# Performance work log

Hardware: AMD Instinct MI355X
Metric: run time of the kernel (lower is better)

The kernel has to match this reference:

```python
import jax, jax.numpy as jnp
import numpy as np

D_IN, D_MODEL = 512, 256
B, N = 2, 512


def setup_inputs() -> dict:
    key = jax.random.key(0)
    ks = jax.random.split(key, 8)
    xav_x = float(np.sqrt(2.0 / (D_IN + D_MODEL)))
    xav_p = float(np.sqrt(2.0 / (4 + D_MODEL)))
    return {
        "x": jax.random.normal(ks[0], (B, N, D_IN), dtype=jnp.float32),
        "pos": jax.random.normal(ks[1], (B, N, 4), dtype=jnp.float32),
        "attn_mask": jax.random.randint(ks[2], (B, N, N), 0, 2, dtype=jnp.int32),
        "Wx": jax.random.normal(ks[3], (D_IN, D_MODEL), dtype=jnp.float32) * xav_x,
        "bx": jnp.zeros((D_MODEL,), dtype=jnp.float32),
        "Wp": jax.random.normal(ks[4], (4, D_MODEL), dtype=jnp.float32) * xav_p,
        "bp": jnp.zeros((D_MODEL,), dtype=jnp.float32),
        "w": jax.random.normal(ks[5], (D_MODEL,), dtype=jnp.float32) * 0.05,
    }


def reference(x, pos, attn_mask, Wx, bx, Wp, bp, w):
    # projected, activated inputs: [B, N, d_model]
    h = jnp.tanh(x @ Wx + bx)
    # pairwise relative positions: [B, N, N, 4]
    rel = pos[:, :, None, :] - pos[:, None, :, :]
    # position MLP + tanh: [B, N, N, d_model]
    z = jnp.tanh(rel @ Wp + bp)
    # scores via dot with weight vector: [B, N, N]
    attn = jnp.einsum("bijd,d->bij", z, w)
    mask = attn_mask != 0
    attn = jnp.where(mask, attn, -jnp.inf)
    attn = jax.nn.softmax(attn, axis=2)
    attn = jnp.where(mask, attn, 0.0)
    # dropout is identity in eval mode
    # weighted sum: [B, N, d_model]
    output = jnp.einsum("bij,bjd->bid", attn, h)
    return (output, attn)
```

## Files before the change

### kernel.cpp

```cpp
#include <hip/hip_runtime.h>
#include <hip/hip_bf16.h>
#include <math.h>

#define BATCH   2
#define SEQ     512
#define DIN     512
#define DM      256

#define LOG2E2  2.88539008177792681f

#if __has_builtin(__builtin_amdgcn_exp2f)
#define EXP2(x) __builtin_amdgcn_exp2f(x)
#else
#define EXP2(x) exp2f(x)
#endif
#if __has_builtin(__builtin_amdgcn_rcpf)
#define RCP(x) __builtin_amdgcn_rcpf(x)
#else
#define RCP(x) (1.0f / (x))
#endif

__device__ __forceinline__ float tanh_from_scaled(float targ) {
    return fmaf(-2.0f, RCP(1.0f + EXP2(targ)), 1.0f);
}

__global__ __launch_bounds__(512) void produce_k(
    const float* __restrict__ pos,
    const float* __restrict__ Wp,
    const float* __restrict__ x,
    const float* __restrict__ Wx,
    const float* __restrict__ bx,
    float4* __restrict__ EB4,
    float* __restrict__ h)
{
    const int tid = threadIdx.x;

    if (blockIdx.x < 128) {
        const int b  = blockIdx.x >> 6;
        const int q  = blockIdx.x & 63;
        const int d0 = 4 * q;
        const float4 p = ((const float4*)pos)[b * SEQ + tid];
        float e[4];
        #pragma unroll
        for (int i = 0; i < 4; i++) {
            const int d = d0 + i;
            const float P = fmaf(p.x, Wp[d], fmaf(p.y, Wp[DM + d],
                            fmaf(p.z, Wp[2*DM + d], p.w * Wp[3*DM + d])));
            e[i] = EXP2(-LOG2E2 * P);
        }
        EB4[((size_t)(b * 64 + q)) * SEQ + tid] = make_float4(e[0], e[1], e[2], e[3]);
        return;
    }

    __shared__ float s_xt[32][68];
    __shared__ float s_wt[64][64];

    const int idx = blockIdx.x - 128;
    const int rt  = idx >> 2;
    const int ct  = idx & 3;
    const int ty  = tid >> 4;
    const int tx  = tid & 15;
    const int row = rt * 32 + ty;
    const int dcol = ct * 64 + 4 * tx;

    float4 acc = make_float4(0.f, 0.f, 0.f, 0.f);

    for (int ks = 0; ks < 8; ks++) {
        const int k0 = ks * 64;
        {
            const int r = tid >> 4, c = tid & 15;
            *(float4*)&s_xt[r][4 * c] =
                *(const float4*)(x + (size_t)(rt * 32 + r) * DIN + k0 + 4 * c);
        }
        #pragma unroll
        for (int s = 0; s < 2; s++) {
            const int fidx = s * 512 + tid;
            const int r = fidx >> 4, c = fidx & 15;
            *(float4*)&s_wt[r][4 * c] =
                *(const float4*)(Wx + (size_t)(k0 + r) * DM + ct * 64 + 4 * c);
        }
        __syncthreads();

        #pragma unroll 8
        for (int k = 0; k < 64; k++) {
            const float  xv = s_xt[ty][k];
            const float4 wq = *(const float4*)&s_wt[k][4 * tx];
            acc.x = fmaf(xv, wq.x, acc.x);
            acc.y = fmaf(xv, wq.y, acc.y);
            acc.z = fmaf(xv, wq.z, acc.z);
            acc.w = fmaf(xv, wq.w, acc.w);
        }
        __syncthreads();
    }

    const float4 bq = *(const float4*)(bx + dcol);
    float4 t;
    t.x = tanh_from_scaled(LOG2E2 * (acc.x + bq.x));
    t.y = tanh_from_scaled(LOG2E2 * (acc.y + bq.y));
    t.z = tanh_from_scaled(LOG2E2 * (acc.z + bq.z));
    t.w = tanh_from_scaled(LOG2E2 * (acc.w + bq.w));
    *(float4*)(h + (size_t)row * DM + dcol) = t;
}

__global__ __launch_bounds__(512) void attend_k(
    const float* __restrict__ pos,
    const float* __restrict__ Wp,
    const float* __restrict__ bp,
    const int*   __restrict__ mask,
    const float* __restrict__ wv,
    const float4* __restrict__ EB4,
    const float* __restrict__ h,
    float* __restrict__ out,
    float* __restrict__ attn_out)
{
    const int b   = blockIdx.x >> 8;
    const int i0  = (blockIdx.x & 255) * 2;
    const int tid = threadIdx.x;
    const int l   = tid & 63;

    __shared__ float4 s_eaA[64], s_eaB[64];
    __shared__ float  s_p[2][SEQ];
    __shared__ float  s_red[2][8];
    __shared__ float  s_o[7][2][DM];

    {
        const int rr = __builtin_amdgcn_readfirstlane(tid >> 8);
        const int d  = tid & 255;
        const float4 p = ((const float4*)pos)[b * SEQ + i0 + rr];
        const float P = fmaf(p.x, Wp[d],
                        fmaf(p.y, Wp[DM + d],
                        fmaf(p.z, Wp[2*DM + d],
                             p.w * Wp[3*DM + d])));
        const float ea = EXP2(LOG2E2 * (P + bp[d]));
        ((float*)(rr ? s_eaB : s_eaA))[d] = ea;
    }
    __syncthreads();

    const float4* __restrict__ EBj = EB4 + (size_t)b * 64 * SEQ + tid;

    float aA = 0.f, aB = 0.f;
    #pragma unroll 8
    for (int q = 0; q < 64; q++) {
        const float4 eb = EBj[(size_t)q * SEQ];
        const float4 eA = s_eaA[q];
        const float4 eB = s_eaB[q];
        const float4 wq = *(const float4*)(wv + 4 * q);

        const float yA0 = fmaf(eA.x, eb.x, 1.0f);
        const float yA1 = fmaf(eA.y, eb.y, 1.0f);
        const float yA2 = fmaf(eA.z, eb.z, 1.0f);
        const float yA3 = fmaf(eA.w, eb.w, 1.0f);
        aA = fmaf(fmaf(wq.y, yA0, wq.x * yA1), RCP(yA0 * yA1), aA);
        aA = fmaf(fmaf(wq.w, yA2, wq.z * yA3), RCP(yA2 * yA3), aA);

        const float yB0 = fmaf(eB.x, eb.x, 1.0f);
        const float yB1 = fmaf(eB.y, eb.y, 1.0f);
        const float yB2 = fmaf(eB.z, eb.z, 1.0f);
        const float yB3 = fmaf(eB.w, eb.w, 1.0f);
        aB = fmaf(fmaf(wq.y, yB0, wq.x * yB1), RCP(yB0 * yB1), aB);
        aB = fmaf(fmaf(wq.w, yB2, wq.z * yB3), RCP(yB2 * yB3), aB);
    }

    const size_t mrowA = (size_t)b * SEQ * SEQ + (size_t)i0 * SEQ + tid;
    const int mA = mask[mrowA];
    const int mB = mask[mrowA + SEQ];
    float pA = mA ? EXP2(-LOG2E2 * aA) : 0.f;
    float pB = mB ? EXP2(-LOG2E2 * aB) : 0.f;

    float sA = pA, sB = pB;
    #pragma unroll
    for (int off = 32; off; off >>= 1) {
        sA += __shfl_xor(sA, off, 64);
        sB += __shfl_xor(sB, off, 64);
    }
    if (l == 0) { s_red[0][tid >> 6] = sA; s_red[1][tid >> 6] = sB; }
    __syncthreads();

    const float4 ra = ((const float4*)s_red[0])[0], rb = ((const float4*)s_red[0])[1];
    const float4 rc = ((const float4*)s_red[1])[0], rd = ((const float4*)s_red[1])[1];
    pA *= __fdividef(1.0f, (ra.x+ra.y+ra.z+ra.w) + (rb.x+rb.y+rb.z+rb.w));
    pB *= __fdividef(1.0f, (rc.x+rc.y+rc.z+rc.w) + (rd.x+rd.y+rd.z+rd.w));

    attn_out[mrowA]       = pA;
    attn_out[mrowA + SEQ] = pB;
    s_p[0][tid] = pA;
    s_p[1][tid] = pB;
    __syncthreads();

    const int dq = tid & 63;
    const int js = __builtin_amdgcn_readfirstlane(tid >> 6);
    const float* __restrict__ hp = h + (size_t)(b * SEQ + js * 64) * DM + 4 * dq;
    const float* __restrict__ p0 = &s_p[0][js * 64];
    const float* __restrict__ p1 = &s_p[1][js * 64];

    float4 a0 = make_float4(0,0,0,0), a1 = a0;
    #pragma unroll 4
    for (int jj = 0; jj < 16; jj++) {
        const float4 P0 = *(const float4*)(p0 + 4 * jj);
        const float4 P1 = *(const float4*)(p1 + 4 * jj);
        const float4 h0 = *(const float4*)(hp + (size_t)(4*jj + 0) * DM);
        const float4 h1 = *(const float4*)(hp + (size_t)(4*jj + 1) * DM);
        const float4 h2 = *(const float4*)(hp + (size_t)(4*jj + 2) * DM);
        const float4 h3 = *(const float4*)(hp + (size_t)(4*jj + 3) * DM);

        a0.x = fmaf(P0.x,h0.x,fmaf(P0.y,h1.x,fmaf(P0.z,h2.x,fmaf(P0.w,h3.x,a0.x))));
        a0.y = fmaf(P0.x,h0.y,fmaf(P0.y,h1.y,fmaf(P0.z,h2.y,fmaf(P0.w,h3.y,a0.y))));
        a0.z = fmaf(P0.x,h0.z,fmaf(P0.y,h1.z,fmaf(P0.z,h2.z,fmaf(P0.w,h3.z,a0.z))));
        a0.w = fmaf(P0.x,h0.w,fmaf(P0.y,h1.w,fmaf(P0.z,h2.w,fmaf(P0.w,h3.w,a0.w))));
        a1.x = fmaf(P1.x,h0.x,fmaf(P1.y,h1.x,fmaf(P1.z,h2.x,fmaf(P1.w,h3.x,a1.x))));
        a1.y = fmaf(P1.x,h0.y,fmaf(P1.y,h1.y,fmaf(P1.z,h2.y,fmaf(P1.w,h3.y,a1.y))));
        a1.z = fmaf(P1.x,h0.z,fmaf(P1.y,h1.z,fmaf(P1.z,h2.z,fmaf(P1.w,h3.z,a1.z))));
        a1.w = fmaf(P1.x,h0.w,fmaf(P1.y,h1.w,fmaf(P1.z,h2.w,fmaf(P1.w,h3.w,a1.w))));
    }

    if (js > 0) {
        *(float4*)&s_o[js - 1][0][4 * dq] = a0;
        *(float4*)&s_o[js - 1][1][4 * dq] = a1;
    }
    __syncthreads();
    if (js == 0) {
        #pragma unroll
        for (int s = 0; s < 7; s++) {
            const float4 q0 = *(const float4*)&s_o[s][0][4 * dq];
            const float4 q1 = *(const float4*)&s_o[s][1][4 * dq];
            a0.x += q0.x; a0.y += q0.y; a0.z += q0.z; a0.w += q0.w;
            a1.x += q1.x; a1.y += q1.y; a1.z += q1.z; a1.w += q1.w;
        }
        float* __restrict__ op = out + (size_t)(b * SEQ + i0) * DM + 4 * dq;
        *(float4*)(op)      = a0;
        *(float4*)(op + DM) = a1;
    }
}

extern "C" void kernel_launch(void* const* d_in, const int* in_sizes, int n_in,
                              void* d_out, int out_size, void* d_ws, size_t ws_size,
                              hipStream_t stream) {
    const float* x    = (const float*)d_in[0];
    const float* pos  = (const float*)d_in[1];
    const int*   mask = (const int*)  d_in[2];
    const float* Wx   = (const float*)d_in[3];
    const float* bx   = (const float*)d_in[4];
    const float* Wp   = (const float*)d_in[5];
    const float* bp   = (const float*)d_in[6];
    const float* wv   = (const float*)d_in[7];

    float* out      = (float*)d_out;
    float* attn_out = (float*)d_out + (size_t)BATCH*SEQ*DM;

    char*   ws  = (char*)d_ws;
    float*  h   = (float*)(ws);
    float4* EB4 = (float4*)(ws + (size_t)BATCH*SEQ*DM*4);

    produce_k<<<256, 512, 0, stream>>>(pos, Wp, x, Wx, bx, EB4, h);
    attend_k <<<(BATCH*SEQ)/2, 512, 0, stream>>>(pos, Wp, bp, mask, wv, EB4, h, out, attn_out);
}
```

Baseline: 114.8 us.

## Process four query rows per block and split Wx GEMM along K

The attend kernel now handles four query rows per block instead of two. Each EB value loaded from global memory is reused across four rows, which halves the number of blocks and halves the global traffic for EB and h. The EB layout changes from float4 per feature group to a scalar per feature, and the inner loop pairs adjacent features differently. The h GEMM in produce_k splits K across two half-blocks with a shared-memory reduction and uses narrower 32-column tiles, giving 256 GEMM blocks instead of 128. The cost is more registers and shared memory per attend block and fewer attend blocks (256) available to fill the GPU.

After: 106.8 us (median of 2 runs). 7.0% less time.

```diff
diff --git a/kernel.cpp b/kernel.cpp
--- a/kernel.cpp
+++ b/kernel.cpp
@@ -30,7 +30,7 @@
     const float* __restrict__ x,
     const float* __restrict__ Wx,
     const float* __restrict__ bx,
-    float4* __restrict__ EB4,
+    float* __restrict__ EBf,
     float* __restrict__ h)
 {
     const int tid = threadIdx.x;
@@ -40,51 +40,53 @@
         const int q  = blockIdx.x & 63;
         const int d0 = 4 * q;
         const float4 p = ((const float4*)pos)[b * SEQ + tid];
-        float e[4];
         #pragma unroll
         for (int i = 0; i < 4; i++) {
             const int d = d0 + i;
             const float P = fmaf(p.x, Wp[d], fmaf(p.y, Wp[DM + d],
                             fmaf(p.z, Wp[2*DM + d], p.w * Wp[3*DM + d])));
-            e[i] = EXP2(-LOG2E2 * P);
-        }
-        EB4[((size_t)(b * 64 + q)) * SEQ + tid] = make_float4(e[0], e[1], e[2], e[3]);
+            EBf[((size_t)(b * DM + d)) * SEQ + tid] = EXP2(-LOG2E2 * P);
+        }
         return;
     }
 
-    __shared__ float s_xt[32][68];
-    __shared__ float s_wt[64][64];
+    __shared__ float  s_xt[2][32][68];
+    __shared__ float  s_wt[2][64][32];
+    __shared__ float4 s_part[256];
 
     const int idx = blockIdx.x - 128;
-    const int rt  = idx >> 2;
-    const int ct  = idx & 3;
-    const int ty  = tid >> 4;
-    const int tx  = tid & 15;
+    const int rt  = idx >> 3;
+    const int ct  = idx & 7;
+    const int kh  = __builtin_amdgcn_readfirstlane(tid >> 8);
+    const int t   = tid & 255;
+    const int ty  = t >> 3;
+    const int tx  = t & 7;
     const int row = rt * 32 + ty;
-    const int dcol = ct * 64 + 4 * tx;
 
     float4 acc = make_float4(0.f, 0.f, 0.f, 0.f);
 
-    for (int ks = 0; ks < 8; ks++) {
-        const int k0 = ks * 64;
-        {
-            const int r = tid >> 4, c = tid & 15;
-            *(float4*)&s_xt[r][4 * c] =
-                *(const float4*)(x + (size_t)(rt * 32 + r) * DIN + k0 + 4 * c);
-        }
+    for (int ks = 0; ks < 4; ks++) {
+        const int k0 = kh * 256 + ks * 64;
         #pragma unroll
         for (int s = 0; s < 2; s++) {
-            const int fidx = s * 512 + tid;
+            const int fidx = t * 2 + s;
             const int r = fidx >> 4, c = fidx & 15;
-            *(float4*)&s_wt[r][4 * c] =
-                *(const float4*)(Wx + (size_t)(k0 + r) * DM + ct * 64 + 4 * c);
+            *(float4*)&s_xt[kh][r][4 * c] =
+                *(const float4*)(x + (size_t)(rt * 32 + r) * DIN + k0 + 4 * c);
+        }
+        #pragma unroll
+        for (int s = 0; s < 2; s++) {
+            const int fidx = t * 2 + s;
+            const int r = fidx >> 3, c = fidx & 7;
+            *(float4*)&s_wt[kh][r][4 * c] =
+                *(const float4*)(Wx + (size_t)(k0 + r) * DM + ct * 32 + 4 * c);
         }
         __syncthreads();
 
         #pragma unroll 8
         for (int k = 0; k < 64; k++) {
-            const float  xv = s_xt[ty][k];
-            const float4 wq = *(const float4*)&s_wt[k][4 * tx];
+            const float  xv = s_xt[kh][ty][k];
+            const float4 wq = *(const float4*)&s_wt[kh][k][4 * tx];
             acc.x = fmaf(xv, wq.x, acc.x);
             acc.y = fmaf(xv, wq.y, acc.y);
             acc.z = fmaf(xv, wq.z, acc.z);
@@ -93,13 +95,18 @@
         __syncthreads();
     }
 
-    const float4 bq = *(const float4*)(bx + dcol);
-    float4 t;
-    t.x = tanh_from_scaled(LOG2E2 * (acc.x + bq.x));
-    t.y = tanh_from_scaled(LOG2E2 * (acc.y + bq.y));
-    t.z = tanh_from_scaled(LOG2E2 * (acc.z + bq.z));
-    t.w = tanh_from_scaled(LOG2E2 * (acc.w + bq.w));
-    *(float4*)(h + (size_t)row * DM + dcol) = t;
+    if (kh == 1) s_part[t] = acc;
+    __syncthreads();
+    if (kh == 0) {
+        const float4 q4 = s_part[t];
+        const float4 bq = *(const float4*)(bx + ct * 32 + 4 * tx);
+        float4 o;
+        o.x = tanh_from_scaled(LOG2E2 * (acc.x + q4.x + bq.x));
+        o.y = tanh_from_scaled(LOG2E2 * (acc.y + q4.y + bq.y));
+        o.z = tanh_from_scaled(LOG2E2 * (acc.z + q4.z + bq.z));
+        o.w = tanh_from_scaled(LOG2E2 * (acc.w + q4.w + bq.w));
+        *(float4*)(h + (size_t)row * DM + ct * 32 + 4 * tx) = o;
+    }
 }
 
 __global__ __launch_bounds__(512) void attend_k(
@@ -108,114 +115,150 @@
     const float* __restrict__ bp,
     const int*   __restrict__ mask,
     const float* __restrict__ wv,
-    const float4* __restrict__ EB4,
+    const float* __restrict__ EBf,
     const float* __restrict__ h,
     float* __restrict__ out,
     float* __restrict__ attn_out)
 {
-    const int b   = blockIdx.x >> 8;
-    const int i0  = (blockIdx.x & 255) * 2;
+    const int b   = blockIdx.x >> 7;
+    const int i0  = (blockIdx.x & 127) * 4;
     const int tid = threadIdx.x;
     const int l   = tid & 63;
 
-    __shared__ float4 s_eaA[64], s_eaB[64];
-    __shared__ float  s_p[2][SEQ];
-    __shared__ float  s_red[2][8];
-    __shared__ float  s_o[7][2][DM];
+    __shared__ float4 s_ea[DM];
+    __shared__ float  s_p[4][SEQ];
+    __shared__ float  s_red[4][8];
+    __shared__ float  s_o[7][4][DM];
 
     {
-        const int rr = __builtin_amdgcn_readfirstlane(tid >> 8);
         const int d  = tid & 255;
-        const float4 p = ((const float4*)pos)[b * SEQ + i0 + rr];
-        const float P = fmaf(p.x, Wp[d],
-                        fmaf(p.y, Wp[DM + d],
-                        fmaf(p.z, Wp[2*DM + d],
-                             p.w * Wp[3*DM + d])));
-        const float ea = EXP2(LOG2E2 * (P + bp[d]));
-        ((float*)(rr ? s_eaB : s_eaA))[d] = ea;
-    }
-    __syncthreads();
-
-    const float4* __restrict__ EBj = EB4 + (size_t)b * 64 * SEQ + tid;
-
-    float aA = 0.f, aB = 0.f;
+        const int rp = __builtin_amdgcn_readfirstlane(tid >> 8);
+        const int r0 = rp * 2;
+        const float4 p0 = ((const float4*)pos)[b * SEQ + i0 + r0];
+        const float4 p1 = ((const float4*)pos)[b * SEQ + i0 + r0 + 1];
+        const float wp0 = Wp[d], wp1 = Wp[DM + d], wp2 = Wp[2*DM + d], wp3 = Wp[3*DM + d];
+        const float bpd = bp[d];
+        const float P0 = fmaf(p0.x, wp0, fmaf(p0.y, wp1, fmaf(p0.z, wp2, p0.w * wp3)));
+        const float P1 = fmaf(p1.x, wp0, fmaf(p1.y, wp1, fmaf(p1.z, wp2, p1.w * wp3)));
+        float* se = (float*)&s_ea[d];
+        se[r0]     = EXP2(LOG2E2 * (P0 + bpd));
+        se[r0 + 1] = EXP2(LOG2E2 * (P1 + bpd));
+    }
+    __syncthreads();
+
+    const float* __restrict__ EBj = EBf + (size_t)b * DM * SEQ + tid;
+
+    float a0 = 0.f, a1 = 0.f, a2 = 0.f, a3 = 0.f;
     #pragma unroll 8
-    for (int q = 0; q < 64; q++) {
-        const float4 eb = EBj[(size_t)q * SEQ];
-        const float4 eA = s_eaA[q];
-        const float4 eB = s_eaB[q];
-        const float4 wq = *(const float4*)(wv + 4 * q);
-
-        const float yA0 = fmaf(eA.x, eb.x, 1.0f);
-        const float yA1 = fmaf(eA.y, eb.y, 1.0f);
-        const float yA2 = fmaf(eA.z, eb.z, 1.0f);
-        const float yA3 = fmaf(eA.w, eb.w, 1.0f);
-        aA = fmaf(fmaf(wq.y, yA0, wq.x * yA1), RCP(yA0 * yA1), aA);
-        aA = fmaf(fmaf(wq.w, yA2, wq.z * yA3), RCP(yA2 * yA3), aA);
-
-        const float yB0 = fmaf(eB.x, eb.x, 1.0f);
-        const float yB1 = fmaf(eB.y, eb.y, 1.0f);
-        const float yB2 = fmaf(eB.z, eb.z, 1.0f);
-        const float yB3 = fmaf(eB.w, eb.w, 1.0f);
-        aB = fmaf(fmaf(wq.y, yB0, wq.x * yB1), RCP(yB0 * yB1), aB);
-        aB = fmaf(fmaf(wq.w, yB2, wq.z * yB3), RCP(yB2 * yB3), aB);
-    }
-
-    const size_t mrowA = (size_t)b * SEQ * SEQ + (size_t)i0 * SEQ + tid;
-    const int mA = mask[mrowA];
-    const int mB = mask[mrowA + SEQ];
-    float pA = mA ? EXP2(-LOG2E2 * aA) : 0.f;
-    float pB = mB ? EXP2(-LOG2E2 * aB) : 0.f;
-
-    float sA = pA, sB = pB;
+    for (int t = 0; t < 128; t++) {
+        const float eb0 = EBj[(size_t)(2*t) * SEQ];
+        const float eb1 = EBj[(size_t)(2*t + 1) * SEQ];
+        const float4 eA = s_ea[2*t];
+        const float4 eB = s_ea[2*t + 1];
+        const float w0 = wv[2*t];
+        const float w1 = wv[2*t + 1];
+
+        {
+            const float y0 = fmaf(eA.x, eb0, 1.f), y1 = fmaf(eB.x, eb1, 1.f);
+            a0 = fmaf(fmaf(w0, y1, w1 * y0), RCP(y0 * y1), a0);
+        }
+        {
+            const float y0 = fmaf(eA.y, eb0, 1.f), y1 = fmaf(eB.y, eb1, 1.f);
+            a1 = fmaf(fmaf(w0, y1, w1 * y0), RCP(y0 * y1), a1);
+        }
+        {
+            const float y0 = fmaf(eA.z, eb0, 1.f), y1 = fmaf(eB.z, eb1, 1.f);
+            a2 = fmaf(fmaf(w0, y1, w1 * y0), RCP(y0 * y1), a2);
+        }
+        {
+            const float y0 = fmaf(eA.w, eb0, 1.f), y1 = fmaf(eB.w, eb1, 1.f);
+            a3 = fmaf(fmaf(w0, y1, w1 * y0), RCP(y0 * y1), a3);
+        }
+    }
+
+    const size_t mrow = (size_t)b * SEQ * SEQ + (size_t)i0 * SEQ + tid;
+    const int m0 = mask[mrow];
+    const int m1 = mask[mrow + SEQ];
+    const int m2 = mask[mrow + 2*SEQ];
+    const int m3 = mask[mrow + 3*SEQ];
+    float p0 = m0 ? EXP2(-LOG2E2 * a0) : 0.f;
+    float p1 = m1 ? EXP2(-LOG2E2 * a1) : 0.f;
+    float p2 = m2 ? EXP2(-LOG2E2 * a2) : 0.f;
+    float p3 = m3 ? EXP2(-LOG2E2 * a3) : 0.f;
+
+    float s0 = p0, s1 = p1, s2 = p2, s3 = p3;
     #pragma unroll
     for (int off = 32; off; off >>= 1) {
-        sA += __shfl_xor(sA, off, 64);
-        sB += __shfl_xor(sB, off, 64);
-    }
-    if (l == 0) { s_red[0][tid >> 6] = sA; s_red[1][tid >> 6] = sB; }
-    __syncthreads();
-
-    const float4 ra = ((const float4*)s_red[0])[0], rb = ((const float4*)s_red[0])[1];
-    const float4 rc = ((const float4*)s_red[1])[0], rd = ((const float4*)s_red[1])[1];
-    pA *= __fdividef(1.0f, (ra.x+ra.y+ra.z+ra.w) + (rb.x+rb.y+rb.z+rb.w));
-    pB *= __fdividef(1.0f, (rc.x+rc.y+rc.z+rc.w) + (rd.x+rd.y+rd.z+rd.w));
-
-    attn_out[mrowA]       = pA;
-    attn_out[mrowA + SEQ] = pB;
-    s_p[0][tid] = pA;
-    s_p[1][tid] = pB;
+        s0 += __shfl_xor(s0, off, 64);
+        s1 += __shfl_xor(s1, off, 64);
+        s2 += __shfl_xor(s2, off, 64);
+        s3 += __shfl_xor(s3, off, 64);
+    }
+    const int w = tid >> 6;
+    if (l == 0) { s_red[0][w] = s0; s_red[1][w] = s1; s_red[2][w] = s2; s_red[3][w] = s3; }
+    __syncthreads();
+
+    {
+        const float4 r0a = ((const float4*)s_red[0])[0], r0b = ((const float4*)s_red[0])[1];
+        const float4 r1a = ((const float4*)s_red[1])[0], r1b = ((const float4*)s_red[1])[1];
+        const float4 r2a = ((const float4*)s_red[2])[0], r2b = ((const float4*)s_red[2])[1];
+        const float4 r3a = ((const float4*)s_red[3])[0], r3b = ((const float4*)s_red[3])[1];
+        p0 *= __fdividef(1.0f, (r0a.x+r0a.y+r0a.z+r0a.w) + (r0b.x+r0b.y+r0b.z+r0b.w));
+        p1 *= __fdividef(1.0f, (r1a.x+r1a.y+r1a.z+r1a.w) + (r1b.x+r1b.y+r1b.z+r1b.w));
+        p2 *= __fdividef(1.0f, (r2a.x+r2a.y+r2a.z+r2a.w) + (r2b.x+r2b.y+r2b.z+r2b.w));
+        p3 *= __fdividef(1.0f, (r3a.x+r3a.y+r3a.z+r3a.w) + (r3b.x+r3b.y+r3b.z+r3b.w));
+    }
+
+    attn_out[mrow]         = p0;
+    attn_out[mrow + SEQ]   = p1;
+    attn_out[mrow + 2*SEQ] = p2;
+    attn_out[mrow + 3*SEQ] = p3;
+    s_p[0][tid] = p0; s_p[1][tid] = p1; s_p[2][tid] = p2; s_p[3][tid] = p3;
     __syncthreads();
 
     const int dq = tid & 63;
     const int js = __builtin_amdgcn_readfirstlane(tid >> 6);
     const float* __restrict__ hp = h + (size_t)(b * SEQ + js * 64) * DM + 4 * dq;
-    const float* __restrict__ p0 = &s_p[0][js * 64];
-    const float* __restrict__ p1 = &s_p[1][js * 64];
-
-    float4 a0 = make_float4(0,0,0,0), a1 = a0;
+    const float* __restrict__ q0p = &s_p[0][js * 64];
+    const float* __restrict__ q1p = &s_p[1][js * 64];
+    const float* __restrict__ q2p = &s_p[2][js * 64];
+    const float* __restrict__ q3p = &s_p[3][js * 64];
+
+    float4 a0v = make_float4(0,0,0,0), a1v = a0v, a2v = a0v, a3v = a0v;
     #pragma unroll 4
     for (int jj = 0; jj < 16; jj++) {
-        const float4 P0 = *(const float4*)(p0 + 4 * jj);
-        const float4 P1 = *(const float4*)(p1 + 4 * jj);
+        const float4 P0 = *(const float4*)(q0p + 4 * jj);
+        const float4 P1 = *(const float4*)(q1p + 4 * jj);
+        const float4 P2 = *(const float4*)(q2p + 4 * jj);
+        const float4 P3 = *(const float4*)(q3p + 4 * jj);
         const float4 h0 = *(const float4*)(hp + (size_t)(4*jj + 0) * DM);
         const float4 h1 = *(const float4*)(hp + (size_t)(4*jj + 1) * DM);
         const float4 h2 = *(const float4*)(hp + (size_t)(4*jj + 2) * DM);
         const float4 h3 = *(const float4*)(hp + (size_t)(4*jj + 3) * DM);
 
-        a0.x = fmaf(P0.x,h0.x,fmaf(P0.y,h1.x,fmaf(P0.z,h2.x,fmaf(P0.w,h3.x,a0.x))));
-        a0.y = fmaf(P0.x,h0.y,fmaf(P0.y,h1.y,fmaf(P0.z,h2.y,fmaf(P0.w,h3.y,a0.y))));
-        a0.z = fmaf(P0.x,h0.z,fmaf(P0.y,h1.z,fmaf(P0.z,h2.z,fmaf(P0.w,h3.z,a0.z))));
-        a0.w = fmaf(P0.x,h0.w,fmaf(P0.y,h1.w,fmaf(P0.z,h2.w,fmaf(P0.w,h3.w,a0.w))));
-        a1.x = fmaf(P1.x,h0.x,fmaf(P1.y,h1.x,fmaf(P1.z,h2.x,fmaf(P1.w,h3.x,a1.x))));
-        a1.y = fmaf(P1.x,h0.y,fmaf(P1.y,h1.y,fmaf(P1.z,h2.y,fmaf(P1.w,h3.y,a1.y))));
-        a1.z = fmaf(P1.x,h0.z,fmaf(P1.y,h1.z,fmaf(P1.z,h2.z,fmaf(P1.w,h3.z,a1.z))));
-        a1.w = fmaf(P1.x,h0.w,fmaf(P1.y,h1.w,fmaf(P1.z,h2.w,fmaf(P1.w,h3.w,a1.w))));
+        a0v.x = fmaf(P0.x,h0.x,fmaf(P0.y,h1.x,fmaf(P0.z,h2.x,fmaf(P0.w,h3.x,a0v.x))));
+        a0v.y = fmaf(P0.x,h0.y,fmaf(P0.y,h1.y,fmaf(P0.z,h2.y,fmaf(P0.w,h3.y,a0v.y))));
+        a0v.z = fmaf(P0.x,h0.z,fmaf(P0.y,h1.z,fmaf(P0.z,h2.z,fmaf(P0.w,h3.z,a0v.z))));
+        a0v.w = fmaf(P0.x,h0.w,fmaf(P0.y,h1.w,fmaf(P0.z,h2.w,fmaf(P0.w,h3.w,a0v.w))));
+        a1v.x = fmaf(P1.x,h0.x,fmaf(P1.y,h1.x,fmaf(P1.z,h2.x,fmaf(P1.w,h3.x,a1v.x))));
+        a1v.y = fmaf(P1.x,h0.y,fmaf(P1.y,h1.y,fmaf(P1.z,h2.y,fmaf(P1.w,h3.y,a1v.y))));
+        a1v.z = fmaf(P1.x,h0.z,fmaf(P1.y,h1.z,fmaf(P1.z,h2.z,fmaf(P1.w,h3.z,a1v.z))));
+        a1v.w = fmaf(P1.x,h0.w,fmaf(P1.y,h1.w,fmaf(P1.z,h2.w,fmaf(P1.w,h3.w,a1v.w))));
+        a2v.x = fmaf(P2.x,h0.x,fmaf(P2.y,h1.x,fmaf(P2.z,h2.x,fmaf(P2.w,h3.x,a2v.x))));
+        a2v.y = fmaf(P2.x,h0.y,fmaf(P2.y,h1.y,fmaf(P2.z,h2.y,fmaf(P2.w,h3.y,a2v.y))));
+        a2v.z = fmaf(P2.x,h0.z,fmaf(P2.y,h1.z,fmaf(P2.z,h2.z,fmaf(P2.w,h3.z,a2v.z))));
+        a2v.w = fmaf(P2.x,h0.w,fmaf(P2.y,h1.w,fmaf(P2.z,h2.w,fmaf(P2.w,h3.w,a2v.w))));
+        a3v.x = fmaf(P3.x,h0.x,fmaf(P3.y,h1.x,fmaf(P3.z,h2.x,fmaf(P3.w,h3.x,a3v.x))));
+        a3v.y = fmaf(P3.x,h0.y,fmaf(P3.y,h1.y,fmaf(P3.z,h2.y,fmaf(P3.w,h3.y,a3v.y))));
+        a3v.z = fmaf(P3.x,h0.z,fmaf(P3.y,h1.z,fmaf(P3.z,h2.z,fmaf(P3.w,h3.z,a3v.z))));
+        a3v.w = fmaf(P3.x,h0.w,fmaf(P3.y,h1.w,fmaf(P3.z,h2.w,fmaf(P3.w,h3.w,a3v.w))));
     }
 
     if (js > 0) {
-        *(float4*)&s_o[js - 1][0][4 * dq] = a0;
-        *(float4*)&s_o[js - 1][1][4 * dq] = a1;
+        *(float4*)&s_o[js - 1][0][4 * dq] = a0v;
+        *(float4*)&s_o[js - 1][1][4 * dq] = a1v;
+        *(float4*)&s_o[js - 1][2][4 * dq] = a2v;
+        *(float4*)&s_o[js - 1][3][4 * dq] = a3v;
     }
     __syncthreads();
     if (js == 0) {
@@ -223,12 +266,18 @@
         for (int s = 0; s < 7; s++) {
             const float4 q0 = *(const float4*)&s_o[s][0][4 * dq];
             const float4 q1 = *(const float4*)&s_o[s][1][4 * dq];
-            a0.x += q0.x; a0.y += q0.y; a0.z += q0.z; a0.w += q0.w;
-            a1.x += q1.x; a1.y += q1.y; a1.z += q1.z; a1.w += q1.w;
+            const float4 q2 = *(const float4*)&s_o[s][2][4 * dq];
+            const float4 q3 = *(const float4*)&s_o[s][3][4 * dq];
+            a0v.x += q0.x; a0v.y += q0.y; a0v.z += q0.z; a0v.w += q0.w;
+            a1v.x += q1.x; a1v.y += q1.y; a1v.z += q1.z; a1v.w += q1.w;
+            a2v.x += q2.x; a2v.y += q2.y; a2v.z += q2.z; a2v.w += q2.w;
+            a3v.x += q3.x; a3v.y += q3.y; a3v.z += q3.z; a3v.w += q3.w;
         }
         float* __restrict__ op = out + (size_t)(b * SEQ + i0) * DM + 4 * dq;
-        *(float4*)(op)      = a0;
-        *(float4*)(op + DM) = a1;
+        *(float4*)(op)        = a0v;
+        *(float4*)(op + DM)   = a1v;
+        *(float4*)(op + 2*DM) = a2v;
+        *(float4*)(op + 3*DM) = a3v;
     }
 }
 
@@ -247,10 +296,10 @@
     float* out      = (float*)d_out;
     float* attn_out = (float*)d_out + (size_t)BATCH*SEQ*DM;
 
-    char*   ws  = (char*)d_ws;
-    float*  h   = (float*)(ws);
-    float4* EB4 = (float4*)(ws + (size_t)BATCH*SEQ*DM*4);
-
-    produce_k<<<256, 512, 0, stream>>>(pos, Wp, x, Wx, bx, EB4, h);
-    attend_k <<<(BATCH*SEQ)/2, 512, 0, stream>>>(pos, Wp, bp, mask, wv, EB4, h, out, attn_out);
+    char*  ws  = (char*)d_ws;
+    float* h   = (float*)(ws);
+    float* EBf = (float*)(ws + (size_t)BATCH*SEQ*DM*4);
+
+    produce_k<<<384, 512, 0, stream>>>(pos, Wp, x, Wx, bx, EBf, h);
+    attend_k <<<(BATCH*SEQ)/4, 512, 0, stream>>>(pos, Wp, bp, mask, wv, EBf, h, out, attn_out);
 }
```
